# Performance work log

Measured on AMD Instinct MI355X. Metric: run time of the kernel, lower is better.

## Reference

```python
import jax, jax.numpy as jnp
import numpy as np

# dims / hyperparams (mirror init_kwargs)
B, N, C, K = 256, 16000, 32, 64          # batch, samples, cochlear channels, gammatone taps
FS, FMIN, FMAX, BWF = 16000, 100.0, 8000.0, 1.0
WINDOW, STRIDE = 256, 128                # inner hair cell framing -> T = 124
ANS, HID, OUT = 10, 50, 10               # auditory-nerve fanout, bushy/ic hidden, AC out
BETA, THR = 0.95, 1.0                    # snn.Leaky(beta=0.95), threshold 1.0, subtract reset
AN_LO, AN_HI, AN_THR = 0.5, 1.5, 0.5     # an_range scales + AN firing threshold

# Heaviside spike with ATan surrogate gradient (snntorch default style)
@jax.custom_vjp
def spike(u):
    return (u > 0).astype(u.dtype)

def _spike_fwd(u):
    return spike(u), u

def _spike_bwd(u, g):
    return (g / (1.0 + (jnp.pi * u) ** 2),)

spike.defvjp(_spike_fwd, _spike_bwd)

def _gammatone_bank():
    # ERB-spaced 4th-order gammatone impulse responses, unit L2 norm. [C, K]
    def hz2erb(f):
        return 21.4 * np.log10(1.0 + 0.00437 * f)
    def erb2hz(e):
        return (10.0 ** (e / 21.4) - 1.0) / 0.00437
    cfs = erb2hz(np.linspace(hz2erb(FMIN), hz2erb(FMAX), C))
    b = BWF * 1.019 * 24.7 * (4.37 * cfs / 1000.0 + 1.0)
    t = np.arange(K) / FS
    ker = (t[None, :] ** 3) * np.exp(-2 * np.pi * b[:, None] * t[None, :]) \
          * np.cos(2 * np.pi * cfs[:, None] * t[None, :])
    ker = ker / (np.linalg.norm(ker, axis=1, keepdims=True) + 1e-12)
    return jnp.asarray(ker, jnp.float32)

def setup_inputs() -> dict:
    key = jax.random.key(0)
    k1, k2, k3, k4 = jax.random.split(key, 4)
    audio = jax.random.normal(k1, (B, N), dtype=jnp.float32)
    W_bushy = jax.random.normal(k2, (HID, C * ANS), dtype=jnp.float32) / np.sqrt(C * ANS)
    W_ic = jax.random.normal(k3, (HID, HID), dtype=jnp.float32) / np.sqrt(HID)
    W_ac = jax.random.normal(k4, (OUT, HID), dtype=jnp.float32) / np.sqrt(HID)
    return {"audio": audio, "gt_kernels": _gammatone_bank(),
            "W_bushy": W_bushy, "W_ic": W_ic, "W_ac": W_ac}

def reference(audio, gt_kernels, W_bushy, W_ic, W_ac):
    # Cochlear: gammatone filterbank, [B,1,N] conv [C,1,K] SAME -> [B,C,N]
    y = jax.lax.conv_general_dilated(audio[:, None, :], gt_kernels[:, None, :],
                                     window_strides=(1,), padding="SAME")
    # InnerHairCell: half-wave rectify + moving-average framing -> [B,C,T]
    y = jnp.maximum(y, 0.0)
    env = jax.lax.reduce_window(y, 0.0, jax.lax.add,
                                (1, 1, WINDOW), (1, 1, STRIDE), "VALID") / WINDOW
    frames = jnp.transpose(env, (2, 0, 1))  # [T,B,C]
    scales = jnp.linspace(AN_LO, AN_HI, ANS, dtype=jnp.float32)

    def lif(mem, cur):
        mem = BETA * mem + cur
        spk = spike(mem - THR)
        return spk, mem - THR * spk  # subtract reset

    def step(carry, x_t):  # x_t [B,C]
        mem_b, mem_ic, mem_ac = carry
        # AuditoryNerve: ans scaled copies per channel, threshold fire -> [B, C*ANS]
        spk_an = spike(x_t[:, :, None] * scales - AN_THR).reshape(x_t.shape[0], -1)
        spk_b, mem_b = lif(mem_b, spk_an @ W_bushy.T)     # Bushy
        spk_ic, mem_ic = lif(mem_ic, spk_b @ W_ic.T)      # InferiorColliculus
        spk_ac, mem_ac = lif(mem_ac, spk_ic @ W_ac.T)     # AudioCortex
        return (mem_b, mem_ic, mem_ac), (spk_ac, mem_ac)

    bsz = audio.shape[0]
    init = (jnp.zeros((bsz, HID), audio.dtype),
            jnp.zeros((bsz, HID), audio.dtype),
            jnp.zeros((bsz, OUT), audio.dtype))
    _, (spk_rec, mem_rec) = jax.lax.scan(step, init, frames)
    # stack along dim=1 as in torch code -> [B,T,OUT]
    return jnp.transpose(spk_rec, (1, 0, 2)), jnp.transpose(mem_rec, (1, 0, 2))
```

## Files before the change

kernel.cpp:

```cpp
#include <hip/hip_runtime.h>

#define B_   256
#define N_   16000
#define C_   32
#define K_   64
#define T_   124
#define NJ   125
#define HID_ 50
#define OUT_ 10
#define TB_  1024
#define CURS 52

typedef unsigned int u32;
typedef float v2f __attribute__((ext_vector_type(2)));
struct __align__(16) f2x2 { v2f lo, hi; };

__device__ __forceinline__ float fadd(float a, float b) { return __fadd_rn(a, b); }
__device__ __forceinline__ float fmul(float a, float b) { return __fmul_rn(a, b); }
__device__ __forceinline__ float fsub(float a, float b) { return __fsub_rn(a, b); }

__device__ __forceinline__ void PKFMA(v2f& y, v2f a, const f2x2& T, int k) {
    switch (k) {
    case 0:  asm("v_pk_fma_f32 %0, %1, %2, %0 op_sel:[0,0,0] op_sel_hi:[1,0,1]"
                 : "+v"(y) : "v"(a), "s"(T.lo)); break;
    case 1:  asm("v_pk_fma_f32 %0, %1, %2, %0 op_sel:[0,1,0] op_sel_hi:[1,1,1]"
                 : "+v"(y) : "v"(a), "s"(T.lo)); break;
    case 2:  asm("v_pk_fma_f32 %0, %1, %2, %0 op_sel:[0,0,0] op_sel_hi:[1,0,1]"
                 : "+v"(y) : "v"(a), "s"(T.hi)); break;
    default: asm("v_pk_fma_f32 %0, %1, %2, %0 op_sel:[0,1,0] op_sel_hi:[1,1,1]"
                 : "+v"(y) : "v"(a), "s"(T.hi)); break;
    }
}

__global__ __launch_bounds__(256, 6) void convA(const float* __restrict__ audio,
                                                const float* __restrict__ gt,
                                                float* __restrict__ Sg) {
    __shared__ __align__(16) float abI[1280];
    __shared__ __align__(16) float ybuf[4][4][272];

    const int b = blockIdx.x, g = blockIdx.y;
    const int tid = threadIdx.x, w = tid >> 6, lane = tid & 63;
    const float* arow = audio + (size_t)b * N_;

    const int origin = (g << 10) - 32;
    for (int idx = tid; idx < 1280; idx += 256) {
        int P = idx / 640, j = idx - P * 640;
        int ii = j >> 1, h = j & 1;
        int gi = origin + (P << 9) + (h << 8) + ii;
        float v = (gi >= 0 && gi < N_) ? arow[gi] : 0.0f;
        abI[P * 640 + (j ^ (((j >> 5) & 1) << 2))] = v;
    }
    __syncthreads();

#pragma unroll 1
    for (int P = 0; P < 2; ++P) {
        const float* abP = abI + P * 640;
#pragma unroll 1
        for (int G = 0; G < 2; ++G) {
            const int rowbase = __builtin_amdgcn_readfirstlane(((w << 3) + (G << 2)) << 6);
            const float* kg = gt + rowbase;

            v2f Y[4][4];
#pragma unroll
            for (int ch = 0; ch < 4; ++ch)
#pragma unroll
                for (int d = 0; d < 4; ++d) { Y[ch][d].x = 0.0f; Y[ch][d].y = 0.0f; }

            {
                f2x2 Tc[4];
#pragma unroll
                for (int ch = 0; ch < 4; ++ch)
                    Tc[ch] = *(const f2x2*)(kg + (ch << 6));
                const int u = lane;
                const int p1 = (u << 3) ^ (((u >> 2) & 1) << 2);
                const f2x2 A0 = *(const f2x2*)(abP + p1);
                const f2x2 A1 = *(const f2x2*)(abP + (p1 ^ 4));
#pragma unroll
                for (int e = 0; e < 4; ++e) {
                    const v2f a = (e == 0) ? A0.lo : (e == 1) ? A0.hi
                                : (e == 2) ? A1.lo : A1.hi;
#pragma unroll
                    for (int ch = 0; ch < 4; ++ch)
#pragma unroll
                        for (int d = 0; d < 4; ++d) {
                            const int kb = e - 1 - d;
                            if (kb >= 0) PKFMA(Y[ch][d], a, Tc[ch], kb);
                        }
                }
            }

#pragma unroll 1
            for (int q = 1; q < 16; ++q) {
                f2x2 Tm[4], Tc[4];
#pragma unroll
                for (int ch = 0; ch < 4; ++ch) {
                    Tm[ch] = *(const f2x2*)(kg + (ch << 6) + ((q - 1) << 2));
                    Tc[ch] = *(const f2x2*)(kg + (ch << 6) + (q << 2));
                }
                const int u = lane + q;
                const int p1 = (u << 3) ^ (((u >> 2) & 1) << 2);
                const f2x2 A0 = *(const f2x2*)(abP + p1);
                const f2x2 A1 = *(const f2x2*)(abP + (p1 ^ 4));
#pragma unroll
                for (int e = 0; e < 4; ++e) {
                    const v2f a = (e == 0) ? A0.lo : (e == 1) ? A0.hi
                                : (e == 2) ? A1.lo : A1.hi;
#pragma unroll
                    for (int ch = 0; ch < 4; ++ch)
#pragma unroll
                        for (int d = 0; d < 4; ++d) {
                            const int ts = e - 1 - d;
                            if (ts >= 0) PKFMA(Y[ch][d], a, Tc[ch], ts);
                            else         PKFMA(Y[ch][d], a, Tm[ch], 4 + ts);
                        }
                }
            }

            {
                f2x2 Tm[4];
#pragma unroll
                for (int ch = 0; ch < 4; ++ch)
                    Tm[ch] = *(const f2x2*)(kg + (ch << 6) + 60);
                const int u = lane + 16;
                const int p1 = (u << 3) ^ (((u >> 2) & 1) << 2);
                const f2x2 A0 = *(const f2x2*)(abP + p1);
                const f2x2 A1 = *(const f2x2*)(abP + (p1 ^ 4));
#pragma unroll
                for (int e = 0; e < 4; ++e) {
                    const v2f a = (e == 0) ? A0.lo : (e == 1) ? A0.hi
                                : (e == 2) ? A1.lo : A1.hi;
#pragma unroll
                    for (int ch = 0; ch < 4; ++ch)
#pragma unroll
                        for (int d = 0; d < 4; ++d) {
                            const int ts = e - 1 - d;
                            if (ts < 0) PKFMA(Y[ch][d], a, Tm[ch], 4 + ts);
                        }
                }
            }

#pragma unroll
            for (int h = 0; h < 2; ++h) {
                const int pp = (P << 1) + h;
#pragma unroll
                for (int ch = 0; ch < 4; ++ch) {
                    float4 z;
                    z.x = fmaxf(h ? Y[ch][0].y : Y[ch][0].x, 0.0f);
                    z.y = fmaxf(h ? Y[ch][1].y : Y[ch][1].x, 0.0f);
                    z.z = fmaxf(h ? Y[ch][2].y : Y[ch][2].x, 0.0f);
                    z.w = fmaxf(h ? Y[ch][3].y : Y[ch][3].x, 0.0f);
                    *(float4*)(&ybuf[w][ch][((lane >> 5) * 136) + ((lane & 31) << 2)]) = z;
                }
                {
                    const int ch2 = lane >> 4, blk = (lane >> 3) & 1, j = lane & 7;
                    const float* yb = &ybuf[w][ch2][blk * 136 + j];
                    float r = yb[0];
#pragma unroll
                    for (int m = 1; m < 16; ++m) r = fadd(r, yb[m << 3]);
                    float v = fadd(r, __shfl_xor(r, 1));
                    v = fadd(v, __shfl_xor(v, 2));
                    v = fadd(v, __shfl_xor(v, 4));
                    const int jg = (g << 3) + (pp << 1) + blk;
                    const int c = (w << 3) + (G << 2) + ch2;
                    if (j == 0 && jg < NJ) Sg[((size_t)b * C_ + c) * NJ + jg] = v;
                }
            }
        }
    }
}

__global__ __launch_bounds__(TB_, 1) void snnB(const float* __restrict__ Sg,
                                               const float* __restrict__ Wb,
                                               const float* __restrict__ Wic,
                                               const float* __restrict__ Wac,
                                               float* __restrict__ out) {
    __shared__ float sWb[HID_ * 321];
    __shared__ __align__(16) float sWic[HID_ * 52];
    __shared__ __align__(16) float sWac[OUT_ * 52];
    __shared__ u32   mask[128 * 10];
    __shared__ __align__(16) float cur[T_ * CURS];
    __shared__ __align__(16) float icur[T_ * CURS];
    __shared__ float acur[T_ * 12];

    const int b = blockIdx.x, tid = threadIdx.x;

    for (int i = tid; i < HID_ * 320; i += TB_) {
        int r = i / 320;
        sWb[r * 321 + (i - r * 320)] = Wb[i];
    }
    for (int i = tid; i < HID_ * HID_; i += TB_) {
        int r = i / 50;
        sWic[r * 52 + (i - r * 50)] = Wic[i];
    }
    for (int i = tid; i < OUT_ * HID_; i += TB_) {
        int r = i / 50;
        sWac[r * 52 + (i - r * 50)] = Wac[i];
    }

    const float* Sb = Sg + (size_t)b * C_ * NJ;
    for (int idx = tid; idx < 1280; idx += TB_) {
        if (idx >= T_ * 10) { mask[idx] = 0; continue; }
        int t = idx / 10, wd = idx - t * 10;
        u32 m = 0;
        int c_prev = -1;
        float env = 0.0f;
        for (int k = 0; k < 32; ++k) {
            int i = wd * 32 + k;
            int c = i / 10, s = i - c * 10;
            if (c != c_prev) {
                env = fmul(fadd(Sb[c * NJ + t], Sb[c * NJ + t + 1]), 0.00390625f);
                c_prev = c;
            }
            float sf = (s == 9) ? 1.5f : (float)(0.5 + (double)s * (1.0 / 9.0));
            if (fsub(fmul(env, sf), 0.5f) > 0.0f) m |= (1u << k);
        }
        mask[idx] = m;
    }
    __syncthreads();

    if (tid < 16 * HID_) {
        const int t0 = tid / 50, h = tid - t0 * 50;
        const float* wr = sWb + h * 321;
        const u32* mrow = mask + t0 * 10;
        v2f A0v = {0.0f, 0.0f}, A1v = {0.0f, 0.0f};
        v2f A2v = {0.0f, 0.0f}, A3v = {0.0f, 0.0f};
#pragma unroll 1
        for (int wi = 0; wi < 10; ++wi) {
            const u32 w0 = mrow[wi], w1 = mrow[160 + wi];
            const u32 w2 = mrow[320 + wi], w3 = mrow[480 + wi];
            const u32 w4 = mrow[640 + wi], w5 = mrow[800 + wi];
            const u32 w6 = mrow[960 + wi], w7 = mrow[1120 + wi];
#pragma unroll
            for (int b2 = 0; b2 < 32; ++b2) {
                const float wv = wr[(wi << 5) + b2];
                const int iw = __float_as_int(wv);
                v2f p0, p1, p2, p3;
                p0.x = __int_as_float(iw & __builtin_amdgcn_sbfe((int)w0, b2, 1));
                p0.y = __int_as_float(iw & __builtin_amdgcn_sbfe((int)w1, b2, 1));
                p1.x = __int_as_float(iw & __builtin_amdgcn_sbfe((int)w2, b2, 1));
                p1.y = __int_as_float(iw & __builtin_amdgcn_sbfe((int)w3, b2, 1));
                p2.x = __int_as_float(iw & __builtin_amdgcn_sbfe((int)w4, b2, 1));
                p2.y = __int_as_float(iw & __builtin_amdgcn_sbfe((int)w5, b2, 1));
                p3.x = __int_as_float(iw & __builtin_amdgcn_sbfe((int)w6, b2, 1));
                p3.y = __int_as_float(iw & __builtin_amdgcn_sbfe((int)w7, b2, 1));
                A0v = A0v + p0;
                A1v = A1v + p1;
                A2v = A2v + p2;
                A3v = A3v + p3;
            }
        }
        cur[(t0      ) * CURS + h] = A0v.x;
        cur[(t0 + 16 ) * CURS + h] = A0v.y;
        cur[(t0 + 32 ) * CURS + h] = A1v.x;
        cur[(t0 + 48 ) * CURS + h] = A1v.y;
        cur[(t0 + 64 ) * CURS + h] = A2v.x;
        cur[(t0 + 80 ) * CURS + h] = A2v.y;
        cur[(t0 + 96 ) * CURS + h] = A3v.x;
        if (t0 + 112 < T_) cur[(t0 + 112) * CURS + h] = A3v.y;
    }
    __syncthreads();

    if (tid < HID_) {
        float mem = 0.0f;
        for (int t0 = 0; t0 < 120; t0 += 8) {
            float c0[8];
#pragma unroll
            for (int k = 0; k < 8; ++k) c0[k] = cur[(t0 + k) * CURS + tid];
#pragma unroll
            for (int k = 0; k < 8; ++k) {
                float m = fadd(fmul(0.95f, mem), c0[k]);
                float sp = (fsub(m, 1.0f) > 0.0f) ? 1.0f : 0.0f;
                mem = fsub(m, sp);
                cur[(t0 + k) * CURS + tid] = sp;
            }
        }
        for (int t = 120; t < T_; ++t) {
            float m = fadd(fmul(0.95f, mem), cur[t * CURS + tid]);
            float sp = (fsub(m, 1.0f) > 0.0f) ? 1.0f : 0.0f;
            mem = fsub(m, sp);
            cur[t * CURS + tid] = sp;
        }
    }
    __syncthreads();

    for (int idx = tid; idx < T_ * 25; idx += TB_) {
        int t = idx / 25, hp = idx - t * 25;
        const float* w0 = sWic + hp * 52;
        const float* w1 = sWic + (hp + 25) * 52;
        const float* sb = cur + t * CURS;
        float acc0 = 0.0f, acc1 = 0.0f;
#pragma unroll
        for (int g4 = 0; g4 < 12; ++g4) {
            const float4 s4 = *(const float4*)(sb + (g4 << 2));
            const float4 wa = *(const float4*)(w0 + (g4 << 2));
            const float4 wb = *(const float4*)(w1 + (g4 << 2));
            acc0 = fmaf(s4.x, wa.x, acc0);  acc1 = fmaf(s4.x, wb.x, acc1);
            acc0 = fmaf(s4.y, wa.y, acc0);  acc1 = fmaf(s4.y, wb.y, acc1);
            acc0 = fmaf(s4.z, wa.z, acc0);  acc1 = fmaf(s4.z, wb.z, acc1);
            acc0 = fmaf(s4.w, wa.w, acc0);  acc1 = fmaf(s4.w, wb.w, acc1);
        }
        acc0 = fmaf(sb[48], w0[48], acc0);  acc1 = fmaf(sb[48], w1[48], acc1);
        acc0 = fmaf(sb[49], w0[49], acc0);  acc1 = fmaf(sb[49], w1[49], acc1);
        icur[t * CURS + hp] = acc0;
        icur[t * CURS + hp + 25] = acc1;
    }
    __syncthreads();

    if (tid < HID_) {
        float mem = 0.0f;
        for (int t0 = 0; t0 < 120; t0 += 8) {
            float c0[8];
#pragma unroll
            for (int k = 0; k < 8; ++k) c0[k] = icur[(t0 + k) * CURS + tid];
#pragma unroll
            for (int k = 0; k < 8; ++k) {
                float m = fadd(fmul(0.95f, mem), c0[k]);
                float sp = (fsub(m, 1.0f) > 0.0f) ? 1.0f : 0.0f;
                mem = fsub(m, sp);
                icur[(t0 + k) * CURS + tid] = sp;
            }
        }
        for (int t = 120; t < T_; ++t) {
            float m = fadd(fmul(0.95f, mem), icur[t * CURS + tid]);
            float sp = (fsub(m, 1.0f) > 0.0f) ? 1.0f : 0.0f;
            mem = fsub(m, sp);
            icur[t * CURS + tid] = sp;
        }
    }
    __syncthreads();

    for (int idx = tid; idx < T_ * 5; idx += TB_) {
        int t = idx / 5, op = idx - t * 5;
        const float* w0 = sWac + op * 52;
        const float* w1 = sWac + (op + 5) * 52;
        const float* sb = icur + t * CURS;
        float acc0 = 0.0f, acc1 = 0.0f;
#pragma unroll
        for (int g4 = 0; g4 < 12; ++g4) {
            const float4 s4 = *(const float4*)(sb + (g4 << 2));
            const float4 wa = *(const float4*)(w0 + (g4 << 2));
            const float4 wb = *(const float4*)(w1 + (g4 << 2));
            acc0 = fmaf(s4.x, wa.x, acc0);  acc1 = fmaf(s4.x, wb.x, acc1);
            acc0 = fmaf(s4.y, wa.y, acc0);  acc1 = fmaf(s4.y, wb.y, acc1);
            acc0 = fmaf(s4.z, wa.z, acc0);  acc1 = fmaf(s4.z, wb.z, acc1);
            acc0 = fmaf(s4.w, wa.w, acc0);  acc1 = fmaf(s4.w, wb.w, acc1);
        }
        acc0 = fmaf(sb[48], w0[48], acc0);  acc1 = fmaf(sb[48], w1[48], acc1);
        acc0 = fmaf(sb[49], w0[49], acc0);  acc1 = fmaf(sb[49], w1[49], acc1);
        acur[t * 12 + op] = acc0;
        acur[t * 12 + op + 5] = acc1;
    }
    __syncthreads();

    if (tid < OUT_) {
        float mem = 0.0f;
        for (int t0 = 0; t0 < 120; t0 += 8) {
            float c0[8];
#pragma unroll
            for (int k = 0; k < 8; ++k) c0[k] = acur[(t0 + k) * 12 + tid];
#pragma unroll
            for (int k = 0; k < 8; ++k) {
                float m = fadd(fmul(0.95f, mem), c0[k]);
                float sp = (fsub(m, 1.0f) > 0.0f) ? 1.0f : 0.0f;
                float mo = fsub(m, sp);
                mem = mo;
                size_t base = ((size_t)b * T_ + (t0 + k)) * OUT_ + tid;
                out[base] = sp;
                out[(size_t)(B_ * T_ * OUT_) + base] = mo;
            }
        }
        for (int t = 120; t < T_; ++t) {
            float m = fadd(fmul(0.95f, mem), acur[t * 12 + tid]);
            float sp = (fsub(m, 1.0f) > 0.0f) ? 1.0f : 0.0f;
            float mo = fsub(m, sp);
            mem = mo;
            size_t base = ((size_t)b * T_ + t) * OUT_ + tid;
            out[base] = sp;
            out[(size_t)(B_ * T_ * OUT_) + base] = mo;
        }
    }
}

extern "C" void kernel_launch(void* const* d_in, const int* in_sizes, int n_in,
                              void* d_out, int out_size, void* d_ws, size_t ws_size,
                              hipStream_t stream) {
    (void)in_sizes; (void)n_in; (void)out_size; (void)ws_size;
    const float* audio = (const float*)d_in[0];
    const float* gt    = (const float*)d_in[1];
    const float* Wb    = (const float*)d_in[2];
    const float* Wic   = (const float*)d_in[3];
    const float* Wac   = (const float*)d_in[4];

    float* Sg = (float*)d_ws;

    convA<<<dim3(B_, 16), dim3(256), 0, stream>>>(audio, gt, Sg);
    snnB<<<dim3(B_), dim3(TB_), 0, stream>>>(Sg, Wb, Wic, Wac, (float*)d_out);
}
```

Before: 308.4 us.

## Pipeline SNN layer recurrences across time chunks and merge conv halves per pass

```diff
diff --git a/kernel.cpp b/kernel.cpp
--- a/kernel.cpp
+++ b/kernel.cpp
@@ -32,7 +32,7 @@
     }
 }
 
-__global__ __launch_bounds__(256, 6) void convA(const float* __restrict__ audio,
+__global__ __launch_bounds__(256, 4) void convA(const float* __restrict__ audio,
                                                 const float* __restrict__ gt,
                                                 float* __restrict__ Sg) {
     __shared__ __align__(16) float abI[1280];
@@ -52,27 +52,26 @@
     }
     __syncthreads();
 
-#pragma unroll 1
-    for (int P = 0; P < 2; ++P) {
-        const float* abP = abI + P * 640;
-#pragma unroll 1
-        for (int G = 0; G < 2; ++G) {
-            const int rowbase = __builtin_amdgcn_readfirstlane(((w << 3) + (G << 2)) << 6);
-            const float* kg = gt + rowbase;
-
-            v2f Y[4][4];
-#pragma unroll
-            for (int ch = 0; ch < 4; ++ch)
-#pragma unroll
-                for (int d = 0; d < 4; ++d) { Y[ch][d].x = 0.0f; Y[ch][d].y = 0.0f; }
-
-            {
-                f2x2 Tc[4];
-#pragma unroll
-                for (int ch = 0; ch < 4; ++ch)
-                    Tc[ch] = *(const f2x2*)(kg + (ch << 6));
-                const int u = lane;
-                const int p1 = (u << 3) ^ (((u >> 2) & 1) << 2);
+    for (int G = 0; G < 2; ++G) {
+        const int rowbase = __builtin_amdgcn_readfirstlane(((w << 3) + (G << 2)) << 6);
+        const float* kg = gt + rowbase;
+
+        v2f Y[2][4][4];
+#pragma unroll
+        for (int P = 0; P < 2; ++P)
+#pragma unroll
+            for (int ch = 0; ch < 4; ++ch)
+#pragma unroll
+                for (int d = 0; d < 4; ++d) { Y[P][ch][d].x = 0.0f; Y[P][ch][d].y = 0.0f; }
+
+        f2x2 Ta[4], Tb[4];
+
+        auto BODY = [&](int q, const f2x2* TM, const f2x2* TC) {
+            const int u = lane + q;
+            const int p1 = (u << 3) ^ (((u >> 2) & 1) << 2);
+#pragma unroll
+            for (int P = 0; P < 2; ++P) {
+                const float* abP = abI + P * 640;
                 const f2x2 A0 = *(const f2x2*)(abP + p1);
                 const f2x2 A1 = *(const f2x2*)(abP + (p1 ^ 4));
 #pragma unroll
@@ -83,22 +82,23 @@
                     for (int ch = 0; ch < 4; ++ch)
 #pragma unroll
                         for (int d = 0; d < 4; ++d) {
-                            const int kb = e - 1 - d;
-                            if (kb >= 0) PKFMA(Y[ch][d], a, Tc[ch], kb);
+                            const int ts = e - 1 - d;
+                            if (ts >= 0) PKFMA(Y[P][ch][d], a, TC[ch], ts);
+                            else         PKFMA(Y[P][ch][d], a, TM[ch], 4 + ts);
                         }
                 }
             }
-
-#pragma unroll 1
-            for (int q = 1; q < 16; ++q) {
-                f2x2 Tm[4], Tc[4];
-#pragma unroll
-                for (int ch = 0; ch < 4; ++ch) {
-                    Tm[ch] = *(const f2x2*)(kg + (ch << 6) + ((q - 1) << 2));
-                    Tc[ch] = *(const f2x2*)(kg + (ch << 6) + (q << 2));
-                }
-                const int u = lane + q;
-                const int p1 = (u << 3) ^ (((u >> 2) & 1) << 2);
+        };
+
+        {
+#pragma unroll
+            for (int ch = 0; ch < 4; ++ch)
+                Ta[ch] = *(const f2x2*)(kg + (ch << 6));
+            const int u = lane;
+            const int p1 = (u << 3) ^ (((u >> 2) & 1) << 2);
+#pragma unroll
+            for (int P = 0; P < 2; ++P) {
+                const float* abP = abI + P * 640;
                 const f2x2 A0 = *(const f2x2*)(abP + p1);
                 const f2x2 A1 = *(const f2x2*)(abP + (p1 ^ 4));
 #pragma unroll
@@ -109,20 +109,38 @@
                     for (int ch = 0; ch < 4; ++ch)
 #pragma unroll
                         for (int d = 0; d < 4; ++d) {
-                            const int ts = e - 1 - d;
-                            if (ts >= 0) PKFMA(Y[ch][d], a, Tc[ch], ts);
-                            else         PKFMA(Y[ch][d], a, Tm[ch], 4 + ts);
+                            const int kb = e - 1 - d;
+                            if (kb >= 0) PKFMA(Y[P][ch][d], a, Ta[ch], kb);
                         }
                 }
             }
-
-            {
-                f2x2 Tm[4];
-#pragma unroll
-                for (int ch = 0; ch < 4; ++ch)
-                    Tm[ch] = *(const f2x2*)(kg + (ch << 6) + 60);
-                const int u = lane + 16;
-                const int p1 = (u << 3) ^ (((u >> 2) & 1) << 2);
+        }
+
+#pragma unroll 1
+        for (int qq = 1; qq < 15; qq += 2) {
+#pragma unroll
+            for (int ch = 0; ch < 4; ++ch)
+                Tb[ch] = *(const f2x2*)(kg + (ch << 6) + (qq << 2));
+            BODY(qq, Ta, Tb);
+#pragma unroll
+            for (int ch = 0; ch < 4; ++ch)
+                Ta[ch] = *(const f2x2*)(kg + (ch << 6) + ((qq + 1) << 2));
+            BODY(qq + 1, Tb, Ta);
+        }
+
+        {
+#pragma unroll
+            for (int ch = 0; ch < 4; ++ch)
+                Tb[ch] = *(const f2x2*)(kg + (ch << 6) + 60);
+            BODY(15, Ta, Tb);
+        }
+
+        {
+            const int u = lane + 16;
+            const int p1 = (u << 3) ^ (((u >> 2) & 1) << 2);
+#pragma unroll
+            for (int P = 0; P < 2; ++P) {
+                const float* abP = abI + P * 640;
                 const f2x2 A0 = *(const f2x2*)(abP + p1);
                 const f2x2 A1 = *(const f2x2*)(abP + (p1 ^ 4));
 #pragma unroll
@@ -134,36 +152,36 @@
 #pragma unroll
                         for (int d = 0; d < 4; ++d) {
                             const int ts = e - 1 - d;
-                            if (ts < 0) PKFMA(Y[ch][d], a, Tm[ch], 4 + ts);
+                            if (ts < 0) PKFMA(Y[P][ch][d], a, Tb[ch], 4 + ts);
                         }
                 }
             }
-
-#pragma unroll
-            for (int h = 0; h < 2; ++h) {
-                const int pp = (P << 1) + h;
-#pragma unroll
-                for (int ch = 0; ch < 4; ++ch) {
-                    float4 z;
-                    z.x = fmaxf(h ? Y[ch][0].y : Y[ch][0].x, 0.0f);
-                    z.y = fmaxf(h ? Y[ch][1].y : Y[ch][1].x, 0.0f);
-                    z.z = fmaxf(h ? Y[ch][2].y : Y[ch][2].x, 0.0f);
-                    z.w = fmaxf(h ? Y[ch][3].y : Y[ch][3].x, 0.0f);
-                    *(float4*)(&ybuf[w][ch][((lane >> 5) * 136) + ((lane & 31) << 2)]) = z;
-                }
-                {
-                    const int ch2 = lane >> 4, blk = (lane >> 3) & 1, j = lane & 7;
-                    const float* yb = &ybuf[w][ch2][blk * 136 + j];
-                    float r = yb[0];
-#pragma unroll
-                    for (int m = 1; m < 16; ++m) r = fadd(r, yb[m << 3]);
-                    float v = fadd(r, __shfl_xor(r, 1));
-                    v = fadd(v, __shfl_xor(v, 2));
-                    v = fadd(v, __shfl_xor(v, 4));
-                    const int jg = (g << 3) + (pp << 1) + blk;
-                    const int c = (w << 3) + (G << 2) + ch2;
-                    if (j == 0 && jg < NJ) Sg[((size_t)b * C_ + c) * NJ + jg] = v;
-                }
+        }
+
+#pragma unroll
+        for (int pp = 0; pp < 4; ++pp) {
+            const int P = pp >> 1, h = pp & 1;
+#pragma unroll
+            for (int ch = 0; ch < 4; ++ch) {
+                float4 z;
+                z.x = fmaxf(h ? Y[P][ch][0].y : Y[P][ch][0].x, 0.0f);
+                z.y = fmaxf(h ? Y[P][ch][1].y : Y[P][ch][1].x, 0.0f);
+                z.z = fmaxf(h ? Y[P][ch][2].y : Y[P][ch][2].x, 0.0f);
+                z.w = fmaxf(h ? Y[P][ch][3].y : Y[P][ch][3].x, 0.0f);
+                *(float4*)(&ybuf[w][ch][((lane >> 5) * 136) + ((lane & 31) << 2)]) = z;
+            }
+            {
+                const int ch2 = lane >> 4, blk = (lane >> 3) & 1, j = lane & 7;
+                const float* yb = &ybuf[w][ch2][blk * 136 + j];
+                float r = yb[0];
+#pragma unroll
+                for (int m = 1; m < 16; ++m) r = fadd(r, yb[m << 3]);
+                float v = fadd(r, __shfl_xor(r, 1));
+                v = fadd(v, __shfl_xor(v, 2));
+                v = fadd(v, __shfl_xor(v, 4));
+                const int jg = (g << 3) + (pp << 1) + blk;
+                const int c = (w << 3) + (G << 2) + ch2;
+                if (j == 0 && jg < NJ) Sg[((size_t)b * C_ + c) * NJ + jg] = v;
             }
         }
     }
@@ -260,124 +278,102 @@
     }
     __syncthreads();
 
-    if (tid < HID_) {
-        float mem = 0.0f;
-        for (int t0 = 0; t0 < 120; t0 += 8) {
-            float c0[8];
-#pragma unroll
-            for (int k = 0; k < 8; ++k) c0[k] = cur[(t0 + k) * CURS + tid];
-#pragma unroll
-            for (int k = 0; k < 8; ++k) {
-                float m = fadd(fmul(0.95f, mem), c0[k]);
+    float memB = 0.0f, memI = 0.0f, memA = 0.0f;
+#pragma unroll 1
+    for (int s = 0; s < 8; ++s) {
+        if (s < 4 && tid >= 914 && tid < 964) {
+            const int h = tid - 914, tb = s * 31;
+            float cc[31];
+#pragma unroll
+            for (int k = 0; k < 31; ++k) cc[k] = cur[(tb + k) * CURS + h];
+#pragma unroll
+            for (int k = 0; k < 31; ++k) {
+                float m = fadd(fmul(0.95f, memB), cc[k]);
                 float sp = (fsub(m, 1.0f) > 0.0f) ? 1.0f : 0.0f;
-                mem = fsub(m, sp);
-                cur[(t0 + k) * CURS + tid] = sp;
-            }
-        }
-        for (int t = 120; t < T_; ++t) {
-            float m = fadd(fmul(0.95f, mem), cur[t * CURS + tid]);
-            float sp = (fsub(m, 1.0f) > 0.0f) ? 1.0f : 0.0f;
-            mem = fsub(m, sp);
-            cur[t * CURS + tid] = sp;
-        }
-    }
-    __syncthreads();
-
-    for (int idx = tid; idx < T_ * 25; idx += TB_) {
-        int t = idx / 25, hp = idx - t * 25;
-        const float* w0 = sWic + hp * 52;
-        const float* w1 = sWic + (hp + 25) * 52;
-        const float* sb = cur + t * CURS;
-        float acc0 = 0.0f, acc1 = 0.0f;
-#pragma unroll
-        for (int g4 = 0; g4 < 12; ++g4) {
-            const float4 s4 = *(const float4*)(sb + (g4 << 2));
-            const float4 wa = *(const float4*)(w0 + (g4 << 2));
-            const float4 wb = *(const float4*)(w1 + (g4 << 2));
-            acc0 = fmaf(s4.x, wa.x, acc0);  acc1 = fmaf(s4.x, wb.x, acc1);
-            acc0 = fmaf(s4.y, wa.y, acc0);  acc1 = fmaf(s4.y, wb.y, acc1);
-            acc0 = fmaf(s4.z, wa.z, acc0);  acc1 = fmaf(s4.z, wb.z, acc1);
-            acc0 = fmaf(s4.w, wa.w, acc0);  acc1 = fmaf(s4.w, wb.w, acc1);
-        }
-        acc0 = fmaf(sb[48], w0[48], acc0);  acc1 = fmaf(sb[48], w1[48], acc1);
-        acc0 = fmaf(sb[49], w0[49], acc0);  acc1 = fmaf(sb[49], w1[49], acc1);
-        icur[t * CURS + hp] = acc0;
-        icur[t * CURS + hp + 25] = acc1;
-    }
-    __syncthreads();
-
-    if (tid < HID_) {
-        float mem = 0.0f;
-        for (int t0 = 0; t0 < 120; t0 += 8) {
-            float c0[8];
-#pragma unroll
-            for (int k = 0; k < 8; ++k) c0[k] = icur[(t0 + k) * CURS + tid];
-#pragma unroll
-            for (int k = 0; k < 8; ++k) {
-                float m = fadd(fmul(0.95f, mem), c0[k]);
+                memB = fsub(m, sp);
+                cur[(tb + k) * CURS + h] = sp;
+            }
+        }
+        if (s >= 1 && s <= 4 && tid < 760) {
+            const int tb = (s - 1) * 31;
+            for (int idx = tid; idx < 775; idx += 760) {
+                int tl = idx / 25, hp = idx - tl * 25;
+                int t = tb + tl;
+                const float* w0 = sWic + hp * 52;
+                const float* w1 = sWic + (hp + 25) * 52;
+                const float* sb = cur + t * CURS;
+                float acc0 = 0.0f, acc1 = 0.0f;
+#pragma unroll
+                for (int g4 = 0; g4 < 12; ++g4) {
+                    const float4 s4 = *(const float4*)(sb + (g4 << 2));
+                    const float4 wa = *(const float4*)(w0 + (g4 << 2));
+                    const float4 wb = *(const float4*)(w1 + (g4 << 2));
+                    acc0 = fmaf(s4.x, wa.x, acc0);  acc1 = fmaf(s4.x, wb.x, acc1);
+                    acc0 = fmaf(s4.y, wa.y, acc0);  acc1 = fmaf(s4.y, wb.y, acc1);
+                    acc0 = fmaf(s4.z, wa.z, acc0);  acc1 = fmaf(s4.z, wb.z, acc1);
+                    acc0 = fmaf(s4.w, wa.w, acc0);  acc1 = fmaf(s4.w, wb.w, acc1);
+                }
+                acc0 = fmaf(sb[48], w0[48], acc0);  acc1 = fmaf(sb[48], w1[48], acc1);
+                acc0 = fmaf(sb[49], w0[49], acc0);  acc1 = fmaf(sb[49], w1[49], acc1);
+                icur[t * CURS + hp] = acc0;
+                icur[t * CURS + hp + 25] = acc1;
+            }
+        }
+        if (s >= 2 && s <= 5 && tid >= 964 && tid < 1014) {
+            const int h = tid - 964, tb = (s - 2) * 31;
+            float cc[31];
+#pragma unroll
+            for (int k = 0; k < 31; ++k) cc[k] = icur[(tb + k) * CURS + h];
+#pragma unroll
+            for (int k = 0; k < 31; ++k) {
+                float m = fadd(fmul(0.95f, memI), cc[k]);
                 float sp = (fsub(m, 1.0f) > 0.0f) ? 1.0f : 0.0f;
-                mem = fsub(m, sp);
-                icur[(t0 + k) * CURS + tid] = sp;
-            }
-        }
-        for (int t = 120; t < T_; ++t) {
-            float m = fadd(fmul(0.95f, mem), icur[t * CURS + tid]);
-            float sp = (fsub(m, 1.0f) > 0.0f) ? 1.0f : 0.0f;
-            mem = fsub(m, sp);
-            icur[t * CURS + tid] = sp;
-        }
-    }
-    __syncthreads();
-
-    for (int idx = tid; idx < T_ * 5; idx += TB_) {
-        int t = idx / 5, op = idx - t * 5;
-        const float* w0 = sWac + op * 52;
-        const float* w1 = sWac + (op + 5) * 52;
-        const float* sb = icur + t * CURS;
-        float acc0 = 0.0f, acc1 = 0.0f;
-#pragma unroll
-        for (int g4 = 0; g4 < 12; ++g4) {
-            const float4 s4 = *(const float4*)(sb + (g4 << 2));
-            const float4 wa = *(const float4*)(w0 + (g4 << 2));
-            const float4 wb = *(const float4*)(w1 + (g4 << 2));
-            acc0 = fmaf(s4.x, wa.x, acc0);  acc1 = fmaf(s4.x, wb.x, acc1);
-            acc0 = fmaf(s4.y, wa.y, acc0);  acc1 = fmaf(s4.y, wb.y, acc1);
-            acc0 = fmaf(s4.z, wa.z, acc0);  acc1 = fmaf(s4.z, wb.z, acc1);
-            acc0 = fmaf(s4.w, wa.w, acc0);  acc1 = fmaf(s4.w, wb.w, acc1);
-        }
-        acc0 = fmaf(sb[48], w0[48], acc0);  acc1 = fmaf(sb[48], w1[48], acc1);
-        acc0 = fmaf(sb[49], w0[49], acc0);  acc1 = fmaf(sb[49], w1[49], acc1);
-        acur[t * 12 + op] = acc0;
-        acur[t * 12 + op + 5] = acc1;
-    }
-    __syncthreads();
-
-    if (tid < OUT_) {
-        float mem = 0.0f;
-        for (int t0 = 0; t0 < 120; t0 += 8) {
-            float c0[8];
-#pragma unroll
-            for (int k = 0; k < 8; ++k) c0[k] = acur[(t0 + k) * 12 + tid];
-#pragma unroll
-            for (int k = 0; k < 8; ++k) {
-                float m = fadd(fmul(0.95f, mem), c0[k]);
+                memI = fsub(m, sp);
+                icur[(tb + k) * CURS + h] = sp;
+            }
+        }
+        if (s >= 3 && s <= 6 && tid >= 760 && tid < 914) {
+            const int tb = (s - 3) * 31;
+            for (int idx = tid - 760; idx < 155; idx += 154) {
+                int tl = idx / 5, op = idx - tl * 5;
+                int t = tb + tl;
+                const float* w0 = sWac + op * 52;
+                const float* w1 = sWac + (op + 5) * 52;
+                const float* sb = icur + t * CURS;
+                float acc0 = 0.0f, acc1 = 0.0f;
+#pragma unroll
+                for (int g4 = 0; g4 < 12; ++g4) {
+                    const float4 s4 = *(const float4*)(sb + (g4 << 2));
+                    const float4 wa = *(const float4*)(w0 + (g4 << 2));
+                    const float4 wb = *(const float4*)(w1 + (g4 << 2));
+                    acc0 = fmaf(s4.x, wa.x, acc0);  acc1 = fmaf(s4.x, wb.x, acc1);
+                    acc0 = fmaf(s4.y, wa.y, acc0);  acc1 = fmaf(s4.y, wb.y, acc1);
+                    acc0 = fmaf(s4.z, wa.z, acc0);  acc1 = fmaf(s4.z, wb.z, acc1);
+                    acc0 = fmaf(s4.w, wa.w, acc0);  acc1 = fmaf(s4.w, wb.w, acc1);
+                }
+                acc0 = fmaf(sb[48], w0[48], acc0);  acc1 = fmaf(sb[48], w1[48], acc1);
+                acc0 = fmaf(sb[49], w0[49], acc0);  acc1 = fmaf(sb[49], w1[49], acc1);
+                acur[t * 12 + op] = acc0;
+                acur[t * 12 + op + 5] = acc1;
+            }
+        }
+        if (s >= 4 && tid >= 1014) {
+            const int o = tid - 1014, tb = (s - 4) * 31;
+            float cc[31];
+#pragma unroll
+            for (int k = 0; k < 31; ++k) cc[k] = acur[(tb + k) * 12 + o];
+#pragma unroll
+            for (int k = 0; k < 31; ++k) {
+                float m = fadd(fmul(0.95f, memA), cc[k]);
                 float sp = (fsub(m, 1.0f) > 0.0f) ? 1.0f : 0.0f;
                 float mo = fsub(m, sp);
-                mem = mo;
-                size_t base = ((size_t)b * T_ + (t0 + k)) * OUT_ + tid;
+                memA = mo;
+                size_t base = ((size_t)b * T_ + (tb + k)) * OUT_ + o;
                 out[base] = sp;
                 out[(size_t)(B_ * T_ * OUT_) + base] = mo;
             }
         }
-        for (int t = 120; t < T_; ++t) {
-            float m = fadd(fmul(0.95f, mem), acur[t * 12 + tid]);
-            float sp = (fsub(m, 1.0f) > 0.0f) ? 1.0f : 0.0f;
-            float mo = fsub(m, sp);
-            mem = mo;
-            size_t base = ((size_t)b * T_ + t) * OUT_ + tid;
-            out[base] = sp;
-            out[(size_t)(B_ * T_ * OUT_) + base] = mo;
-        }
+        __syncthreads();
     }
 }
 
```

Result: slower. 315.9 us (+2.5%).
